# Kernel optimization log

Measured on AMD Instinct MI355X. Metric: run time of the kernel, lower is better.

The kernel has to match this reference:

```python
import jax, jax.numpy as jnp
import numpy as np

N_GROUP = 8
TOPK_GROUP = 4
TOP_K = 8
ROUTED_SCALING_FACTOR = 2.5


def setup_inputs() -> dict:
    key = jax.random.key(0)
    ks = jax.random.split(key, 6)
    T, H, I, E = 256, 1024, 512, 32
    x = jax.random.normal(ks[0], (T, H), dtype=jnp.float32)
    gate_w = jax.random.normal(ks[1], (H, E), dtype=jnp.float32) * 0.05
    e_score_bias = jax.random.normal(ks[2], (E,), dtype=jnp.float32) * 0.05
    Wg = jax.random.normal(ks[3], (E, H, I), dtype=jnp.float32) * 0.02
    Wu = jax.random.normal(ks[4], (E, H, I), dtype=jnp.float32) * 0.02
    Wd = jax.random.normal(ks[5], (E, I, H), dtype=jnp.float32) * 0.02
    return {"x": x, "gate_w": gate_w, "e_score_bias": e_score_bias,
            "Wg": Wg, "Wu": Wu, "Wd": Wd}


def _route_ds3(x, gate_w, e_score_bias):
    # DeepSeek-V3 group-limited top-k routing (routing_ds3 in source).
    T = x.shape[0]
    E = gate_w.shape[1]
    logits = x @ gate_w                      # [T, E]
    scores = jax.nn.sigmoid(logits)
    scores_for_choice = scores + e_score_bias[None, :]
    gsz = E // N_GROUP
    grouped = scores_for_choice.reshape(T, N_GROUP, gsz)
    # group score = sum of top-2 expert scores in group
    group_scores = jnp.sum(jax.lax.top_k(grouped, 2)[0], axis=-1)     # [T, n_group]
    _, group_idx = jax.lax.top_k(group_scores, TOPK_GROUP)            # [T, topk_group]
    rows = jnp.arange(T)[:, None]
    group_mask = jnp.zeros((T, N_GROUP), scores.dtype).at[rows, group_idx].set(1.0)
    score_mask = jnp.repeat(group_mask, gsz, axis=-1)                 # [T, E]
    masked = jnp.where(score_mask > 0, scores_for_choice, 0.0)
    _, topk_idx = jax.lax.top_k(masked, TOP_K)                        # [T, k]
    topk_w = jnp.take_along_axis(scores, topk_idx, axis=1)            # gather raw scores
    topk_w = topk_w / (jnp.sum(topk_w, axis=-1, keepdims=True) + 1e-20)
    topk_w = topk_w * ROUTED_SCALING_FACTOR
    return topk_idx, topk_w


def reference(x, gate_w, e_score_bias, Wg, Wu, Wd):
    T = x.shape[0]
    E = gate_w.shape[1]
    topk_idx, topk_w = _route_ds3(x, gate_w, e_score_bias)
    # dense [T, E] routing-weight matrix (topk indices are unique per row)
    rows = jnp.arange(T)[:, None]
    rw = jnp.zeros((T, E), x.dtype).at[rows, topk_idx].set(topk_w)
    # expert gated MLP (silu), combined with routing weights
    g = jnp.einsum('th,ehi->tei', x, Wg)      # [T, E, I]
    u = jnp.einsum('th,ehi->tei', x, Wu)
    a = jax.nn.silu(g) * u
    y = jnp.einsum('tei,eih->teh', a, Wd)     # [T, E, H]
    out = jnp.einsum('te,teh->th', rw, y)     # weighted combine
    return out
```

## Files before the change

kernel.cpp:

```cpp
#include <hip/hip_runtime.h>
#include <cstdint>
#include <cmath>

constexpr int TT   = 256;
constexpr int HD   = 1024;
constexpr int IDIM = 512;
constexpr int NE   = 32;
constexpr int NGRP = 8;
constexpr int TKG  = 4;
constexpr int TOPK = 8;
constexpr float RSCALE = 2.5f;

constexpr int NSX  = HD / 32;
constexpr int NSA  = IDIM / 32;
constexpr int SLAB = 16 * 64 * 8;

typedef float    f32x4 __attribute__((ext_vector_type(4)));
typedef _Float16 half8 __attribute__((ext_vector_type(8)));

constexpr size_t WS_CNT   = 0;
constexpr size_t WS_TOK   = 256;
constexpr size_t WS_WL    = WS_TOK   + (size_t)NE * TT * 4;
constexpr size_t WS_TSLOT = WS_WL    + (size_t)NE * TT * 4;
constexpr size_t WS_OFFS  = WS_TSLOT + (size_t)TT * TOPK * 4;
constexpr size_t WS_XE    = WS_OFFS  + 256;
constexpr size_t WS_A     = WS_XE + (size_t)NE * NSX * SLAB * 2;

#define GLOAD16(GP, LP) __builtin_amdgcn_global_load_lds(                      \
    (const __attribute__((address_space(1))) unsigned int*)(GP),               \
    (__attribute__((address_space(3))) unsigned int*)(LP), 16, 0, 0)

#define WAITVM(N) asm volatile("s_waitcnt vmcnt(" #N ")" ::: "memory")

__global__ __launch_bounds__(256) void k_route(
    const float* __restrict__ x, const float* __restrict__ gw,
    const float* __restrict__ bias, int* __restrict__ cnt,
    int* __restrict__ tok, float* __restrict__ wl, int* __restrict__ tslot)
{
    int t = blockIdx.x;
    int tid = threadIdx.x;
    int e2 = (tid & 15) * 2;
    int c  = tid >> 4;
    const float* xr = x + (size_t)t * HD;

    float a0 = 0.f, a1 = 0.f;
    int h0 = c * (HD / 16);
#pragma unroll 8
    for (int h = h0; h < h0 + HD / 16; ++h) {
        float xv = xr[h];
        float2 wv = *(const float2*)&gw[(size_t)h * NE + e2];
        a0 += xv * wv.x;
        a1 += xv * wv.y;
    }

    __shared__ float part[16][NE];
    part[c][e2]     = a0;
    part[c][e2 + 1] = a1;
    __syncthreads();

    __shared__ float sc[NE], sfc[NE];
    if (tid < NE) {
        float s = 0.f;
#pragma unroll
        for (int cc = 0; cc < 16; ++cc) s += part[cc][tid];
        float sig = 1.f / (1.f + expf(-s));
        sc[tid]  = sig;
        sfc[tid] = sig + bias[tid];
    }
    __syncthreads();

    if (tid == 0) {
        float gs[NGRP];
        for (int g = 0; g < NGRP; ++g) {
            float m1 = -3.0e38f, m2 = -3.0e38f;
            for (int j = 0; j < 4; ++j) {
                float v = sfc[4 * g + j];
                if (v > m1) { m2 = m1; m1 = v; } else if (v > m2) m2 = v;
            }
            gs[g] = m1 + m2;
        }
        bool gsel[NGRP];
        for (int g = 0; g < NGRP; ++g) gsel[g] = false;
        for (int r = 0; r < TKG; ++r) {
            int bi = -1; float bv = -3.0e38f;
            for (int g = 0; g < NGRP; ++g)
                if (!gsel[g] && gs[g] > bv) { bv = gs[g]; bi = g; }
            gsel[bi] = true;
        }
        float masked[NE];
        for (int i = 0; i < NE; ++i) masked[i] = gsel[i >> 2] ? sfc[i] : 0.0f;
        int   idx[TOPK]; float wv[TOPK]; float wsum = 0.f;
        for (int r = 0; r < TOPK; ++r) {
            int bi = -1; float bv = -3.0e38f;
            for (int i = 0; i < NE; ++i)
                if (masked[i] > bv) { bv = masked[i]; bi = i; }
            masked[bi] = -3.0e38f;
            idx[r] = bi; wv[r] = sc[bi]; wsum += wv[r];
        }
        float inv = RSCALE / (wsum + 1e-20f);
        for (int r = 0; r < TOPK; ++r) {
            int ee = idx[r];
            int pos = atomicAdd(&cnt[ee], 1);
            tok[(size_t)ee * TT + pos] = t;
            wl [(size_t)ee * TT + pos] = wv[r] * inv;
            tslot[t * TOPK + r] = ee * TT + pos;
        }
    }
}

__global__ __launch_bounds__(256) void k_pack(
    const float* __restrict__ x, const int* __restrict__ cnt,
    const int* __restrict__ tok, _Float16* __restrict__ Xe,
    int* __restrict__ offs)
{
    int bid  = blockIdx.x;
    int tid  = threadIdx.x;
    if (bid == 0 && tid == 0) {
        int s = 0;
        for (int e = 0; e < NE; ++e) { offs[e] = s; s += cnt[e]; }
    }
    int xcd  = bid & 7;
    int slot = bid >> 3;
    int e    = xcd * 4 + (slot & 3);
    int s    = slot >> 2;
    int n_e = cnt[e];
    if (n_e == 0) return;
    int w = tid >> 6, lane = tid & 63;
    int m16 = lane & 15, q = lane >> 4;
    _Float16* base = Xe + ((size_t)e * NSX + s) * SLAB;
#pragma unroll
    for (int k = 0; k < 4; ++k) {
        int mt = w + k * 4;
        int slot2 = mt * 16 + m16;
        if (slot2 >= n_e) slot2 = n_e - 1;
        int t = tok[e * TT + slot2];
        const float* src = x + (size_t)t * HD + s * 32 + q * 8;
        f32x4 v0 = *(const f32x4*)src;
        f32x4 v1 = *(const f32x4*)(src + 4);
        half8 h;
        h[0] = (_Float16)v0.x; h[1] = (_Float16)v0.y; h[2] = (_Float16)v0.z; h[3] = (_Float16)v0.w;
        h[4] = (_Float16)v1.x; h[5] = (_Float16)v1.y; h[6] = (_Float16)v1.z; h[7] = (_Float16)v1.w;
        *(half8*)(base + ((size_t)mt * 64 + lane) * 8) = h;
    }
}

__global__ __launch_bounds__(512, 1) void k_gateup(
    const _Float16* __restrict__ Xe, const float* __restrict__ Wg,
    const float* __restrict__ Wu, const int* __restrict__ cnt,
    _Float16* __restrict__ A)
{
    int bid  = blockIdx.x;
    int xcd  = bid & 7;
    int slot = bid >> 3;
    int e    = xcd * 4 + (slot & 3);
    int rest = slot >> 2;
    int ig   = rest & 7;
    int tt   = rest >> 3;
    int n_e = cnt[e];
    if (tt * 128 >= n_e) return;
    int mtbase = tt * 8;
    int tid  = threadIdx.x;
    int w    = tid >> 6;
    int lane = tid & 63;
    int m16 = lane & 15, q = lane >> 4;
    int wr = w & 3, wc = w >> 2;

    __shared__ __align__(16) float    LG[4][32][64];
    __shared__ __align__(16) float    LU[4][32][64];
    __shared__ __align__(16) _Float16 LA[4][4096];

    const _Float16* asrc = Xe + (size_t)e * NSX * SLAB + (size_t)(mtbase + w) * 512 + lane * 8;
    const float* gp = Wg + (size_t)e * HD * IDIM + ig * 64;
    const float* up = Wu + (size_t)e * HD * IDIM + ig * 64;
    int wrow  = 4 * w + (lane >> 4);
    int wcsrc = ((lane & 15) << 2) ^ (((w >> 1) & 1) << 4);

    f32x4 accG[2][2], accU[2][2];
#pragma unroll
    for (int a_ = 0; a_ < 2; ++a_)
#pragma unroll
        for (int b_ = 0; b_ < 2; ++b_) {
            accG[a_][b_] = (f32x4){0.f, 0.f, 0.f, 0.f};
            accU[a_][b_] = (f32x4){0.f, 0.f, 0.f, 0.f};
        }

#define GU_STAGE(B, KS)                                                        \
    { GLOAD16(asrc + (size_t)(KS) * SLAB, &LA[B][w * 512]);                    \
      GLOAD16(gp + ((size_t)(KS) * 32 + wrow) * IDIM + wcsrc, &LG[B][4 * w][0]); \
      GLOAD16(up + ((size_t)(KS) * 32 + wrow) * IDIM + wcsrc, &LU[B][4 * w][0]); }

#define GU_COMPUTE(B)                                                          \
    { int c0 = wc * 32 + (m16 ^ ((q & 1) << 4));                               \
      int c1 = wc * 32 + ((16 + m16) ^ ((q & 1) << 4));                        \
      half8 bg0, bg1, bu0, bu1;                                                \
      _Pragma("unroll")                                                        \
      for (int j_ = 0; j_ < 8; ++j_) {                                         \
        bg0[j_] = (_Float16)LG[B][q * 8 + j_][c0];                             \
        bg1[j_] = (_Float16)LG[B][q * 8 + j_][c1];                             \
        bu0[j_] = (_Float16)LU[B][q * 8 + j_][c0];                             \
        bu1[j_] = (_Float16)LU[B][q * 8 + j_][c1];                             \
      }                                                                        \
      half8 a0 = *(const half8*)&LA[B][wr * 512 + lane * 8];                   \
      half8 a1 = *(const half8*)&LA[B][(wr + 4) * 512 + lane * 8];             \
      __builtin_amdgcn_s_setprio(1);                                           \
      accG[0][0] = __builtin_amdgcn_mfma_f32_16x16x32_f16(a0, bg0, accG[0][0], 0, 0, 0); \
      accG[0][1] = __builtin_amdgcn_mfma_f32_16x16x32_f16(a0, bg1, accG[0][1], 0, 0, 0); \
      accU[0][0] = __builtin_amdgcn_mfma_f32_16x16x32_f16(a0, bu0, accU[0][0], 0, 0, 0); \
      accU[0][1] = __builtin_amdgcn_mfma_f32_16x16x32_f16(a0, bu1, accU[0][1], 0, 0, 0); \
      accG[1][0] = __builtin_amdgcn_mfma_f32_16x16x32_f16(a1, bg0, accG[1][0], 0, 0, 0); \
      accG[1][1] = __builtin_amdgcn_mfma_f32_16x16x32_f16(a1, bg1, accG[1][1], 0, 0, 0); \
      accU[1][0] = __builtin_amdgcn_mfma_f32_16x16x32_f16(a1, bu0, accU[1][0], 0, 0, 0); \
      accU[1][1] = __builtin_amdgcn_mfma_f32_16x16x32_f16(a1, bu1, accU[1][1], 0, 0, 0); \
      __builtin_amdgcn_s_setprio(0); }

    constexpr int NK = HD / 32;
    GU_STAGE(0, 0) GU_STAGE(1, 1) GU_STAGE(2, 2)

#pragma unroll
    for (int ks = 0; ks < NK; ++ks) {
        __builtin_amdgcn_s_barrier();
        if (ks + 3 < NK) GU_STAGE((ks + 3) & 3, ks + 3)
        if      (ks + 4 <= NK) { WAITVM(9); }
        else if (ks + 3 == NK) { WAITVM(6); }
        else if (ks + 2 == NK) { WAITVM(3); }
        else                   { WAITVM(0); }
        __builtin_amdgcn_s_barrier();
        __builtin_amdgcn_sched_barrier(0);
        GU_COMPUTE(ks & 3)
    }
#undef GU_STAGE
#undef GU_COMPUTE

    int sa = ig * 2 + wc;
    _Float16* aout = A + ((size_t)e * NSA + sa) * SLAB;
    int jp = m16 & 7;
#pragma unroll
    for (int mtl = 0; mtl < 2; ++mtl) {
        int mtg = mtbase + wr + 4 * mtl;
#pragma unroll
        for (int cg = 0; cg < 2; ++cg) {
            int qp = cg * 2 + (m16 >> 3);
#pragma unroll
            for (int r = 0; r < 4; ++r) {
                float g = accG[mtl][cg][r], u = accU[mtl][cg][r];
                float a = (g / (1.f + expf(-g))) * u;
                int lanep = qp * 16 + q * 4 + r;
                aout[((size_t)mtg * 64 + lanep) * 8 + jp] = (_Float16)a;
            }
        }
    }
}

__global__ __launch_bounds__(512, 1) void k_down(
    const _Float16* __restrict__ A, const float* __restrict__ Wd,
    const int* __restrict__ cnt, const int* __restrict__ offs,
    const float* __restrict__ wl, float* __restrict__ Y)
{
    int bid  = blockIdx.x;
    int xcd  = bid & 7;
    int slot = bid >> 3;
    int e    = xcd * 4 + (slot & 3);
    int rest = slot >> 2;
    int hg   = rest & 7;
    int tt   = rest >> 3;
    int n_e = cnt[e];
    if (tt * 128 >= n_e) return;
    int mtbase = tt * 8;
    int h0 = hg * 128;
    int tid  = threadIdx.x;
    int w    = tid >> 6;
    int lane = tid & 63;
    int m16 = lane & 15, q = lane >> 4;
    int wr = w & 3, wc = w >> 2;

    __shared__ __align__(16) float    LD[4][32][128];
    __shared__ __align__(16) _Float16 LA[4][4096];

    const _Float16* asrc = A + (size_t)e * NSA * SLAB + (size_t)(mtbase + w) * 512 + lane * 8;
    const float* dp = Wd + (size_t)e * IDIM * HD + h0;
    int rA = 2 * w + (lane >> 5);
    int rB = 2 * (w + 8) + (lane >> 5);
    int csA = ((lane & 31) << 2) ^ (((w >> 2) & 1) << 4);
    int csB = ((lane & 31) << 2) ^ ((((w + 8) >> 2) & 1) << 4);

    f32x4 acc[2][4];
#pragma unroll
    for (int a_ = 0; a_ < 2; ++a_)
#pragma unroll
        for (int b_ = 0; b_ < 4; ++b_) acc[a_][b_] = (f32x4){0.f, 0.f, 0.f, 0.f};

#define DN_STAGE(B, KS)                                                        \
    { GLOAD16(asrc + (size_t)(KS) * SLAB, &LA[B][w * 512]);                    \
      GLOAD16(dp + ((size_t)(KS) * 32 + rA) * HD + csA, &LD[B][2 * w][0]);     \
      GLOAD16(dp + ((size_t)(KS) * 32 + rB) * HD + csB, &LD[B][2 * (w + 8)][0]); }

#define DN_COMPUTE(B)                                                          \
    { half8 bd[4];                                                             \
      _Pragma("unroll")                                                        \
      for (int cg = 0; cg < 4; ++cg) {                                         \
        int col = (wc * 2 + (cg >> 1)) * 32 + ((((cg & 1) << 4) + m16) ^ ((q & 1) << 4)); \
        _Pragma("unroll")                                                      \
        for (int j_ = 0; j_ < 8; ++j_) bd[cg][j_] = (_Float16)LD[B][q * 8 + j_][col]; \
      }                                                                        \
      half8 a0 = *(const half8*)&LA[B][wr * 512 + lane * 8];                   \
      half8 a1 = *(const half8*)&LA[B][(wr + 4) * 512 + lane * 8];             \
      __builtin_amdgcn_s_setprio(1);                                           \
      _Pragma("unroll")                                                        \
      for (int cg = 0; cg < 4; ++cg) {                                         \
        acc[0][cg] = __builtin_amdgcn_mfma_f32_16x16x32_f16(a0, bd[cg], acc[0][cg], 0, 0, 0); \
        acc[1][cg] = __builtin_amdgcn_mfma_f32_16x16x32_f16(a1, bd[cg], acc[1][cg], 0, 0, 0); \
      }                                                                        \
      __builtin_amdgcn_s_setprio(0); }

    constexpr int NK = IDIM / 32;
    DN_STAGE(0, 0) DN_STAGE(1, 1) DN_STAGE(2, 2)

#pragma unroll
    for (int ks = 0; ks < NK; ++ks) {
        __builtin_amdgcn_s_barrier();
        if (ks + 3 < NK) DN_STAGE((ks + 3) & 3, ks + 3)
        if      (ks + 4 <= NK) { WAITVM(9); }
        else if (ks + 3 == NK) { WAITVM(6); }
        else if (ks + 2 == NK) { WAITVM(3); }
        else                   { WAITVM(0); }
        __builtin_amdgcn_s_barrier();
        __builtin_amdgcn_sched_barrier(0);
        DN_COMPUTE(ks & 3)
    }
#undef DN_STAGE
#undef DN_COMPUTE

    int oe = offs[e];
#pragma unroll
    for (int mtl = 0; mtl < 2; ++mtl) {
        int mtg = wr + 4 * mtl;
#pragma unroll
        for (int cg = 0; cg < 4; ++cg) {
            int col = h0 + wc * 64 + cg * 16 + m16;
#pragma unroll
            for (int r = 0; r < 4; ++r) {
                int slot2 = tt * 128 + mtg * 16 + q * 4 + r;
                if (slot2 < n_e) {
                    float wt = wl[(size_t)e * TT + slot2];
                    Y[(size_t)(oe + slot2) * HD + col] = wt * acc[mtl][cg][r];
                }
            }
        }
    }
}

__global__ __launch_bounds__(256) void k_combine(
    const float* __restrict__ Y, const int* __restrict__ tslot,
    const int* __restrict__ offs, float* __restrict__ out)
{
    int t = blockIdx.x, tid = threadIdx.x;
    f32x4 s = (f32x4){0.f, 0.f, 0.f, 0.f};
#pragma unroll
    for (int r = 0; r < TOPK; ++r) {
        int ts  = tslot[t * TOPK + r];
        int e   = ts >> 8;
        int pos = ts & 255;
        const float* yp = Y + (size_t)(offs[e] + pos) * HD + tid * 4;
        f32x4 v = *(const f32x4*)yp;
        s.x += v.x; s.y += v.y; s.z += v.z; s.w += v.w;
    }
    *(f32x4*)&out[(size_t)t * HD + tid * 4] = s;
}

extern "C" void kernel_launch(void* const* d_in, const int* in_sizes, int n_in,
                              void* d_out, int out_size, void* d_ws, size_t ws_size,
                              hipStream_t stream) {
    const float* x    = (const float*)d_in[0];
    const float* gw   = (const float*)d_in[1];
    const float* bias = (const float*)d_in[2];
    const float* Wg   = (const float*)d_in[3];
    const float* Wu   = (const float*)d_in[4];
    const float* Wd   = (const float*)d_in[5];
    float* out = (float*)d_out;

    char* ws = (char*)d_ws;
    int*      cnt   = (int*)(ws + WS_CNT);
    int*      tok   = (int*)(ws + WS_TOK);
    float*    wl    = (float*)(ws + WS_WL);
    int*      tslot = (int*)(ws + WS_TSLOT);
    int*      offs  = (int*)(ws + WS_OFFS);
    _Float16* Xe    = (_Float16*)(ws + WS_XE);
    _Float16* A     = (_Float16*)(ws + WS_A);
    float*    Y     = (float*)(ws + WS_XE);

    hipMemsetAsync(ws, 0, 256, stream);

    k_route<<<TT, 256, 0, stream>>>(x, gw, bias, cnt, tok, wl, tslot);
    k_pack<<<NE * NSX, 256, 0, stream>>>(x, cnt, tok, Xe, offs);
    k_gateup<<<512, 512, 0, stream>>>(Xe, Wg, Wu, cnt, A);
    k_down<<<512, 512, 0, stream>>>(A, Wd, cnt, offs, wl, Y);
    k_combine<<<TT, 256, 0, stream>>>(Y, tslot, offs, out);
}
```

Measured before the change: 246.3 us.

## Stage fp32 weights through registers into padded LDS instead of direct global-to-LDS loads

Both expert GEMM kernels now load the fp32 weight tiles with global_load_dwordx4 into a three-slot register ring. The registers are written to LDS with ds_write_b128 one step ahead, while the activation tiles keep using direct global-to-LDS loads. The LDS rows are padded (66 and 130 floats) in place of the XOR swizzle, which is meant to cut bank conflicts on the column-wise fp16 conversion reads. The cost is extra VGPR pressure, an lgkmcnt wait every iteration, and hand-tuned vmcnt counts that must match the new load ordering.

```diff
diff --git a/kernel.cpp b/kernel.cpp
--- a/kernel.cpp
+++ b/kernel.cpp
@@ -30,7 +30,13 @@
     (const __attribute__((address_space(1))) unsigned int*)(GP),               \
     (__attribute__((address_space(3))) unsigned int*)(LP), 16, 0, 0)
 
+#define GLD128(DST, PTR) asm volatile("global_load_dwordx4 %0, %1, off"       \
+    : "=&v"(DST) : "v"(PTR) : "memory")
+#define DSW128(LP, V) asm volatile("ds_write_b128 %0, %1"                     \
+    :: "v"((__attribute__((address_space(3))) float*)(LP)), "v"(V) : "memory")
+
 #define WAITVM(N) asm volatile("s_waitcnt vmcnt(" #N ")" ::: "memory")
+#define LGKM0     asm volatile("s_waitcnt lgkmcnt(0)" ::: "memory")
 
 __global__ __launch_bounds__(256) void k_route(
     const float* __restrict__ x, const float* __restrict__ gw,
@@ -165,15 +171,16 @@
     int m16 = lane & 15, q = lane >> 4;
     int wr = w & 3, wc = w >> 2;
 
-    __shared__ __align__(16) float    LG[4][32][64];
-    __shared__ __align__(16) float    LU[4][32][64];
+    __shared__ __align__(16) float    LG[4][32][66];
+    __shared__ __align__(16) float    LU[4][32][66];
     __shared__ __align__(16) _Float16 LA[4][4096];
 
     const _Float16* asrc = Xe + (size_t)e * NSX * SLAB + (size_t)(mtbase + w) * 512 + lane * 8;
-    const float* gp = Wg + (size_t)e * HD * IDIM + ig * 64;
-    const float* up = Wu + (size_t)e * HD * IDIM + ig * 64;
-    int wrow  = 4 * w + (lane >> 4);
-    int wcsrc = ((lane & 15) << 2) ^ (((w >> 1) & 1) << 4);
+    int wv = w & 3;
+    const float* wsrc = ((w < 4) ? Wg : Wu) + (size_t)e * HD * IDIM + ig * 64;
+    int rbase = 8 * wv;
+    int rlo   = lane >> 4;
+    int csl   = (lane & 15) * 4;
 
     f32x4 accG[2][2], accU[2][2];
 #pragma unroll
@@ -184,24 +191,33 @@
             accU[a_][b_] = (f32x4){0.f, 0.f, 0.f, 0.f};
         }
 
-#define GU_STAGE(B, KS)                                                        \
-    { GLOAD16(asrc + (size_t)(KS) * SLAB, &LA[B][w * 512]);                    \
-      GLOAD16(gp + ((size_t)(KS) * 32 + wrow) * IDIM + wcsrc, &LG[B][4 * w][0]); \
-      GLOAD16(up + ((size_t)(KS) * 32 + wrow) * IDIM + wcsrc, &LU[B][4 * w][0]); }
-
-#define GU_COMPUTE(B)                                                          \
-    { int c0 = wc * 32 + (m16 ^ ((q & 1) << 4));                               \
-      int c1 = wc * 32 + ((16 + m16) ^ ((q & 1) << 4));                        \
+    f32x4 wr0[3], wr1[3];
+
+#define GU_WLOAD(KS, S)                                                        \
+    { const float* p_ = wsrc + (size_t)((KS) * 32 + rbase) * IDIM;             \
+      GLD128(wr0[S], p_ + (size_t)rlo * IDIM + csl);                           \
+      GLD128(wr1[S], p_ + (size_t)(4 + rlo) * IDIM + csl); }
+
+#define GU_WSTORE(KS, S)                                                       \
+    { float (*LWp_)[66] = (w < 4) ? LG[(KS) & 3] : LU[(KS) & 3];               \
+      DSW128(&LWp_[rbase + rlo][csl], wr0[S]);                                 \
+      DSW128(&LWp_[rbase + 4 + rlo][csl], wr1[S]); }
+
+#define GU_AGLOAD(KS) GLOAD16(asrc + (size_t)(KS) * SLAB, &LA[(KS) & 3][w * 512]);
+
+#define GU_COMPUTE(KS)                                                         \
+    { int B_ = (KS) & 3;                                                       \
+      int c0 = wc * 32 + m16, c1 = c0 + 16;                                    \
       half8 bg0, bg1, bu0, bu1;                                                \
       _Pragma("unroll")                                                        \
       for (int j_ = 0; j_ < 8; ++j_) {                                         \
-        bg0[j_] = (_Float16)LG[B][q * 8 + j_][c0];                             \
-        bg1[j_] = (_Float16)LG[B][q * 8 + j_][c1];                             \
-        bu0[j_] = (_Float16)LU[B][q * 8 + j_][c0];                             \
-        bu1[j_] = (_Float16)LU[B][q * 8 + j_][c1];                             \
+        bg0[j_] = (_Float16)LG[B_][q * 8 + j_][c0];                            \
+        bg1[j_] = (_Float16)LG[B_][q * 8 + j_][c1];                            \
+        bu0[j_] = (_Float16)LU[B_][q * 8 + j_][c0];                            \
+        bu1[j_] = (_Float16)LU[B_][q * 8 + j_][c1];                            \
       }                                                                        \
-      half8 a0 = *(const half8*)&LA[B][wr * 512 + lane * 8];                   \
-      half8 a1 = *(const half8*)&LA[B][(wr + 4) * 512 + lane * 8];             \
+      half8 a0 = *(const half8*)&LA[B_][wr * 512 + lane * 8];                  \
+      half8 a1 = *(const half8*)&LA[B_][(wr + 4) * 512 + lane * 8];            \
       __builtin_amdgcn_s_setprio(1);                                           \
       accG[0][0] = __builtin_amdgcn_mfma_f32_16x16x32_f16(a0, bg0, accG[0][0], 0, 0, 0); \
       accG[0][1] = __builtin_amdgcn_mfma_f32_16x16x32_f16(a0, bg1, accG[0][1], 0, 0, 0); \
@@ -214,21 +230,32 @@
       __builtin_amdgcn_s_setprio(0); }
 
     constexpr int NK = HD / 32;
-    GU_STAGE(0, 0) GU_STAGE(1, 1) GU_STAGE(2, 2)
+    GU_WLOAD(0, 0)
+    __builtin_amdgcn_sched_barrier(0);
+    GU_WLOAD(1, 1) GU_AGLOAD(0)
+    __builtin_amdgcn_sched_barrier(0);
+    GU_WLOAD(2, 2) GU_AGLOAD(1)
+    WAITVM(6);
+    GU_WSTORE(0, 0)
 
 #pragma unroll
     for (int ks = 0; ks < NK; ++ks) {
         __builtin_amdgcn_s_barrier();
-        if (ks + 3 < NK) GU_STAGE((ks + 3) & 3, ks + 3)
-        if      (ks + 4 <= NK) { WAITVM(9); }
-        else if (ks + 3 == NK) { WAITVM(6); }
-        else if (ks + 2 == NK) { WAITVM(3); }
+        if (ks + 3 < NK) GU_WLOAD(ks + 3, ks % 3)
+        if (ks + 2 < NK) GU_AGLOAD(ks + 2)
+        if      (ks + 4 <= NK) { WAITVM(6); }
+        else if (ks + 3 == NK) { WAITVM(4); }
+        else if (ks + 2 == NK) { WAITVM(1); }
         else                   { WAITVM(0); }
+        if (ks + 1 < NK) GU_WSTORE(ks + 1, (ks + 1) % 3)
+        LGKM0;
         __builtin_amdgcn_s_barrier();
         __builtin_amdgcn_sched_barrier(0);
-        GU_COMPUTE(ks & 3)
-    }
-#undef GU_STAGE
+        GU_COMPUTE(ks)
+    }
+#undef GU_WLOAD
+#undef GU_WSTORE
+#undef GU_AGLOAD
 #undef GU_COMPUTE
 
     int sa = ig * 2 + wc;
@@ -273,15 +300,13 @@
     int m16 = lane & 15, q = lane >> 4;
     int wr = w & 3, wc = w >> 2;
 
-    __shared__ __align__(16) float    LD[4][32][128];
+    __shared__ __align__(16) float    LD[4][32][130];
     __shared__ __align__(16) _Float16 LA[4][4096];
 
     const _Float16* asrc = A + (size_t)e * NSA * SLAB + (size_t)(mtbase + w) * 512 + lane * 8;
     const float* dp = Wd + (size_t)e * IDIM * HD + h0;
-    int rA = 2 * w + (lane >> 5);
-    int rB = 2 * (w + 8) + (lane >> 5);
-    int csA = ((lane & 31) << 2) ^ (((w >> 2) & 1) << 4);
-    int csB = ((lane & 31) << 2) ^ ((((w + 8) >> 2) & 1) << 4);
+    int rlo = lane >> 5;
+    int csl = (lane & 31) * 4;
 
     f32x4 acc[2][4];
 #pragma unroll
@@ -289,21 +314,31 @@
 #pragma unroll
         for (int b_ = 0; b_ < 4; ++b_) acc[a_][b_] = (f32x4){0.f, 0.f, 0.f, 0.f};
 
-#define DN_STAGE(B, KS)                                                        \
-    { GLOAD16(asrc + (size_t)(KS) * SLAB, &LA[B][w * 512]);                    \
-      GLOAD16(dp + ((size_t)(KS) * 32 + rA) * HD + csA, &LD[B][2 * w][0]);     \
-      GLOAD16(dp + ((size_t)(KS) * 32 + rB) * HD + csB, &LD[B][2 * (w + 8)][0]); }
-
-#define DN_COMPUTE(B)                                                          \
-    { half8 bd[4];                                                             \
+    f32x4 wr0[3], wr1[3];
+
+#define DN_WLOAD(KS, S)                                                        \
+    { const float* p_ = dp + (size_t)((KS) * 32 + 4 * w) * HD;                 \
+      GLD128(wr0[S], p_ + (size_t)rlo * HD + csl);                             \
+      GLD128(wr1[S], p_ + (size_t)(2 + rlo) * HD + csl); }
+
+#define DN_WSTORE(KS, S)                                                       \
+    { float (*LWp_)[130] = LD[(KS) & 3];                                       \
+      DSW128(&LWp_[4 * w + rlo][csl], wr0[S]);                                 \
+      DSW128(&LWp_[4 * w + 2 + rlo][csl], wr1[S]); }
+
+#define DN_AGLOAD(KS) GLOAD16(asrc + (size_t)(KS) * SLAB, &LA[(KS) & 3][w * 512]);
+
+#define DN_COMPUTE(KS)                                                         \
+    { int B_ = (KS) & 3;                                                       \
+      half8 bd[4];                                                             \
       _Pragma("unroll")                                                        \
       for (int cg = 0; cg < 4; ++cg) {                                         \
-        int col = (wc * 2 + (cg >> 1)) * 32 + ((((cg & 1) << 4) + m16) ^ ((q & 1) << 4)); \
+        int col = wc * 64 + cg * 16 + m16;                                     \
         _Pragma("unroll")                                                      \
-        for (int j_ = 0; j_ < 8; ++j_) bd[cg][j_] = (_Float16)LD[B][q * 8 + j_][col]; \
+        for (int j_ = 0; j_ < 8; ++j_) bd[cg][j_] = (_Float16)LD[B_][q * 8 + j_][col]; \
       }                                                                        \
-      half8 a0 = *(const half8*)&LA[B][wr * 512 + lane * 8];                   \
-      half8 a1 = *(const half8*)&LA[B][(wr + 4) * 512 + lane * 8];             \
+      half8 a0 = *(const half8*)&LA[B_][wr * 512 + lane * 8];                  \
+      half8 a1 = *(const half8*)&LA[B_][(wr + 4) * 512 + lane * 8];            \
       __builtin_amdgcn_s_setprio(1);                                           \
       _Pragma("unroll")                                                        \
       for (int cg = 0; cg < 4; ++cg) {                                         \
@@ -313,21 +348,32 @@
       __builtin_amdgcn_s_setprio(0); }
 
     constexpr int NK = IDIM / 32;
-    DN_STAGE(0, 0) DN_STAGE(1, 1) DN_STAGE(2, 2)
+    DN_WLOAD(0, 0)
+    __builtin_amdgcn_sched_barrier(0);
+    DN_WLOAD(1, 1) DN_AGLOAD(0)
+    __builtin_amdgcn_sched_barrier(0);
+    DN_WLOAD(2, 2) DN_AGLOAD(1)
+    WAITVM(6);
+    DN_WSTORE(0, 0)
 
 #pragma unroll
     for (int ks = 0; ks < NK; ++ks) {
         __builtin_amdgcn_s_barrier();
-        if (ks + 3 < NK) DN_STAGE((ks + 3) & 3, ks + 3)
-        if      (ks + 4 <= NK) { WAITVM(9); }
-        else if (ks + 3 == NK) { WAITVM(6); }
-        else if (ks + 2 == NK) { WAITVM(3); }
+        if (ks + 3 < NK) DN_WLOAD(ks + 3, ks % 3)
+        if (ks + 2 < NK) DN_AGLOAD(ks + 2)
+        if      (ks + 4 <= NK) { WAITVM(6); }
+        else if (ks + 3 == NK) { WAITVM(4); }
+        else if (ks + 2 == NK) { WAITVM(1); }
         else                   { WAITVM(0); }
+        if (ks + 1 < NK) DN_WSTORE(ks + 1, (ks + 1) % 3)
+        LGKM0;
         __builtin_amdgcn_s_barrier();
         __builtin_amdgcn_sched_barrier(0);
-        DN_COMPUTE(ks & 3)
-    }
-#undef DN_STAGE
+        DN_COMPUTE(ks)
+    }
+#undef DN_WLOAD
+#undef DN_WSTORE
+#undef DN_AGLOAD
 #undef DN_COMPUTE
 
     int oe = offs[e];
```

Result: no change. 246.0 us (-0.1%).
